# Kernel tuning notes

Measured on AMD Instinct MI355X. Metric: run time of the kernel, lower is better.

The kernel has to match this reference:

```python
import jax, jax.numpy as jnp
import numpy as np

D_K = 64  # head dim; scale = 1/sqrt(d_k)


def setup_inputs() -> dict:
    key = jax.random.key(0)
    kq, kk, kv = jax.random.split(key, 3)
    B, N, M = 16, 2048, 2048
    q = jax.random.normal(kq, (B, N, D_K), dtype=jnp.float32)
    k = jax.random.normal(kk, (B, M, D_K), dtype=jnp.float32)
    v = jax.random.normal(kv, (B, M, D_K), dtype=jnp.float32)
    return {"q": q, "k": k, "v": v}


def reference(q, k, v):
    # attn = softmax(q @ k^T / sqrt(d_k)); dropout is identity in eval mode
    scale = 1.0 / jnp.sqrt(jnp.asarray(D_K, dtype=q.dtype))
    scores = jnp.einsum("bnd,bmd->bnm", q, k) * scale  # (B, n, m)
    attn = jax.nn.softmax(scores, axis=2)
    out = jnp.einsum("bnm,bmd->bnd", attn, v)  # (B, n, d_v)
    return (out, attn)
```

## Files before the change

kernel.cpp:

```cpp
#include <hip/hip_runtime.h>

#define B_ 16
#define N_ 2048
#define M_ 2048
#define D_ 64

typedef short sv8 __attribute__((ext_vector_type(8)));
typedef short sv4 __attribute__((ext_vector_type(4)));
typedef float fv4 __attribute__((ext_vector_type(4)));

__device__ __forceinline__ short f2bf(float x) {
    union { float f; unsigned u; } a; a.f = x;
    unsigned r = a.u + 0x7FFFu + ((a.u >> 16) & 1u);
    return (short)(r >> 16);
}
__device__ __forceinline__ float bf2f(short s) {
    union { float f; unsigned u; } a;
    a.u = ((unsigned)(unsigned short)s) << 16;
    return a.f;
}

__device__ __forceinline__ int pidx(int r, int m) {
    return (r << 11) + ((((m >> 3) ^ (r & 7))) << 3) + (m & 7);
}

__global__ void conv_bf16(const float* __restrict__ in, short* __restrict__ outb) {
    int i = (blockIdx.x * 256 + threadIdx.x) * 4;
    float4 f = *(const float4*)(in + i);
    sv4 o; o[0] = f2bf(f.x); o[1] = f2bf(f.y); o[2] = f2bf(f.z); o[3] = f2bf(f.w);
    *(sv4*)(outb + i) = o;
}

__global__ void conv_vt(const float* __restrict__ v, short* __restrict__ vt) {
    __shared__ short tile[64][65];
    int t = threadIdx.x;
    int b = blockIdx.x >> 5;
    int mt = (blockIdx.x & 31) << 6;
    for (int i = 0; i < 4; ++i) {
        int idx = i * 256 + t;
        int m = idx >> 4;
        int dq = (idx & 15) << 2;
        float4 f = *(const float4*)(v + ((size_t)(b * M_ + mt + m) * D_ + dq));
        tile[m][dq + 0] = f2bf(f.x); tile[m][dq + 1] = f2bf(f.y);
        tile[m][dq + 2] = f2bf(f.z); tile[m][dq + 3] = f2bf(f.w);
    }
    __syncthreads();
    for (int j = 0; j < 2; ++j) {
        int idx = j * 256 + t;
        int d = idx >> 3;
        int mq = (idx & 7) << 3;
        sv4 o0, o1;
        #pragma unroll
        for (int c = 0; c < 4; ++c) o0[c] = tile[mq + c][d];
        #pragma unroll
        for (int c = 0; c < 4; ++c) o1[c] = tile[mq + 4 + c][d];
        short* dst = vt + ((size_t)(b * D_ + d) * M_ + mt + mq);
        *(sv4*)(dst) = o0;
        *(sv4*)(dst + 4) = o1;
    }
}

__global__ __launch_bounds__(256, 2) void attn_main(
    const short* __restrict__ Qb, const short* __restrict__ Kb,
    const short* __restrict__ Vt, float* __restrict__ outp,
    float* __restrict__ attnp)
{
    __shared__ short P[16 * 2048];
    __shared__ float l_sh[4][16];
    __shared__ float rinv_sh[16];

    const int tid = threadIdx.x;
    const int w = tid >> 6;
    const int lane = tid & 63;
    const int r = lane & 15;
    const int g = lane >> 4;

    const int b = blockIdx.x >> 7;
    const int n0 = (blockIdx.x & 127) << 4;

    const short* qbase = Qb + ((b * N_ + n0 + r) * D_ + g * 8);
    sv8 q0 = *(const sv8*)(qbase);
    sv8 q1 = *(const sv8*)(qbase + 32);

    float lpart = 0.f;

    for (int m0 = w * 16; m0 < M_; m0 += 64) {
        const short* kbase = Kb + ((b * M_ + m0 + r) * D_ + g * 8);
        sv8 a0 = *(const sv8*)(kbase);
        sv8 a1 = *(const sv8*)(kbase + 32);
        fv4 acc = {0.f, 0.f, 0.f, 0.f};
        acc = __builtin_amdgcn_mfma_f32_16x16x32_bf16(a0, q0, acc, 0, 0, 0);
        acc = __builtin_amdgcn_mfma_f32_16x16x32_bf16(a1, q1, acc, 0, 0, 0);
        float p0 = __expf(fminf(acc[0] * 0.125f, 80.f));
        float p1 = __expf(fminf(acc[1] * 0.125f, 80.f));
        float p2 = __expf(fminf(acc[2] * 0.125f, 80.f));
        float p3 = __expf(fminf(acc[3] * 0.125f, 80.f));
        lpart += (p0 + p1) + (p2 + p3);
        sv4 pw; pw[0] = f2bf(p0); pw[1] = f2bf(p1); pw[2] = f2bf(p2); pw[3] = f2bf(p3);
        *(sv4*)&P[pidx(r, m0 + g * 4)] = pw;
    }

    lpart += __shfl_xor(lpart, 16, 64);
    lpart += __shfl_xor(lpart, 32, 64);
    if (g == 0) l_sh[w][r] = lpart;
    __syncthreads();
    if (tid < 16) {
        float s = l_sh[0][tid] + l_sh[1][tid] + l_sh[2][tid] + l_sh[3][tid];
        rinv_sh[tid] = 1.f / s;
    }
    __syncthreads();

    const int base_row = b * N_ + n0;
    for (int i = 0; i < 32; ++i) {
        int idx = i * 256 + tid;
        int rr = idx >> 9;
        int mq = (idx & 511) << 2;
        sv4 pv = *(const sv4*)&P[pidx(rr, mq)];
        float ri = rinv_sh[rr];
        float4 o;
        o.x = bf2f(pv[0]) * ri; o.y = bf2f(pv[1]) * ri;
        o.z = bf2f(pv[2]) * ri; o.w = bf2f(pv[3]) * ri;
        *(float4*)(attnp + ((size_t)(base_row + rr) * M_ + mq)) = o;
    }

    fv4 acc = {0.f, 0.f, 0.f, 0.f};
    const short* vbase = Vt + ((size_t)(b * D_ + w * 16 + r) * M_);
    for (int m0 = 0; m0 < M_; m0 += 32) {
        sv8 pa = *(const sv8*)&P[pidx(r, m0 + g * 8)];
        sv8 vb = *(const sv8*)(vbase + m0 + g * 8);
        acc = __builtin_amdgcn_mfma_f32_16x16x32_bf16(pa, vb, acc, 0, 0, 0);
    }
    #pragma unroll
    for (int reg = 0; reg < 4; ++reg) {
        int nr = g * 4 + reg;
        outp[(size_t)(base_row + nr) * D_ + w * 16 + r] = acc[reg] * rinv_sh[nr];
    }
}

extern "C" void kernel_launch(void* const* d_in, const int* in_sizes, int n_in,
                              void* d_out, int out_size, void* d_ws, size_t ws_size,
                              hipStream_t stream) {
    const float* q = (const float*)d_in[0];
    const float* k = (const float*)d_in[1];
    const float* v = (const float*)d_in[2];
    float* outp = (float*)d_out;
    float* attnp = outp + (size_t)B_ * N_ * D_;

    short* Qb = (short*)d_ws;
    short* Kb = Qb + (size_t)B_ * N_ * D_;
    short* Vt = Kb + (size_t)B_ * M_ * D_;

    conv_bf16<<<2048, 256, 0, stream>>>(q, Qb);
    conv_bf16<<<2048, 256, 0, stream>>>(k, Kb);
    conv_vt<<<512, 256, 0, stream>>>(v, Vt);
    attn_main<<<B_ * (N_ / 16), 256, 0, stream>>>(Qb, Kb, Vt, outp, attnp);
}
```

Before: 156.5 us.

## Split attention into row-sum pass and streaming bulk pass with small per-wave LDS tiles

Replaces the single kernel, which buffered a whole 16x2048 probability row block in LDS, with two kernels. The first recomputes QK^T to get the softmax denominators. The second recomputes the scores and streams normalized attention and P@V in 64-column chunks through small double-buffered per-wave LDS tiles, using nontemporal stores. This cuts LDS use so more blocks fit per CU and lets attention-matrix writes interleave with compute, at the cost of computing QK^T twice. It also switches bf16 conversion to the hardware packed-convert instruction and drops the exp clamp.

```diff
diff --git a/kernel.cpp b/kernel.cpp
--- a/kernel.cpp
+++ b/kernel.cpp
@@ -4,6 +4,7 @@
 #define N_ 2048
 #define M_ 2048
 #define D_ 64
+#define SCALE 0.125f
 
 typedef short sv8 __attribute__((ext_vector_type(8)));
 typedef short sv4 __attribute__((ext_vector_type(4)));
@@ -14,21 +15,19 @@
     unsigned r = a.u + 0x7FFFu + ((a.u >> 16) & 1u);
     return (short)(r >> 16);
 }
-__device__ __forceinline__ float bf2f(short s) {
-    union { float f; unsigned u; } a;
-    a.u = ((unsigned)(unsigned short)s) << 16;
-    return a.f;
-}
-
-__device__ __forceinline__ int pidx(int r, int m) {
-    return (r << 11) + ((((m >> 3) ^ (r & 7))) << 3) + (m & 7);
-}
+__device__ __forceinline__ unsigned cvtpk(float lo, float hi) {
+    unsigned r;
+    asm("v_cvt_pk_bf16_f32 %0, %1, %2" : "=v"(r) : "v"(lo), "v"(hi));
+    return r;
+}
+__device__ __forceinline__ float bflo(unsigned u) { return __uint_as_float(u << 16); }
+__device__ __forceinline__ float bfhi(unsigned u) { return __uint_as_float(u & 0xffff0000u); }
 
 __global__ void conv_bf16(const float* __restrict__ in, short* __restrict__ outb) {
     int i = (blockIdx.x * 256 + threadIdx.x) * 4;
     float4 f = *(const float4*)(in + i);
-    sv4 o; o[0] = f2bf(f.x); o[1] = f2bf(f.y); o[2] = f2bf(f.z); o[3] = f2bf(f.w);
-    *(sv4*)(outb + i) = o;
+    uint2 o; o.x = cvtpk(f.x, f.y); o.y = cvtpk(f.z, f.w);
+    *(uint2*)(outb + i) = o;
 }
 
 __global__ void conv_vt(const float* __restrict__ v, short* __restrict__ vt) {
@@ -60,80 +59,127 @@
     }
 }
 
-__global__ __launch_bounds__(256, 2) void attn_main(
+__global__ __launch_bounds__(256) void attn_sums(
     const short* __restrict__ Qb, const short* __restrict__ Kb,
-    const short* __restrict__ Vt, float* __restrict__ outp,
-    float* __restrict__ attnp)
+    float* __restrict__ rinv_g)
 {
-    __shared__ short P[16 * 2048];
-    __shared__ float l_sh[4][16];
-    __shared__ float rinv_sh[16];
-
     const int tid = threadIdx.x;
-    const int w = tid >> 6;
-    const int lane = tid & 63;
-    const int r = lane & 15;
-    const int g = lane >> 4;
-
-    const int b = blockIdx.x >> 7;
-    const int n0 = (blockIdx.x & 127) << 4;
+    const int w = tid >> 6, lane = tid & 63;
+    const int r = lane & 15, g = lane >> 4;
+    const int b = blockIdx.x >> 5;
+    const int n0 = ((blockIdx.x & 31) << 6) + (w << 4);
 
     const short* qbase = Qb + ((b * N_ + n0 + r) * D_ + g * 8);
     sv8 q0 = *(const sv8*)(qbase);
     sv8 q1 = *(const sv8*)(qbase + 32);
-
-    float lpart = 0.f;
-
-    for (int m0 = w * 16; m0 < M_; m0 += 64) {
-        const short* kbase = Kb + ((b * M_ + m0 + r) * D_ + g * 8);
-        sv8 a0 = *(const sv8*)(kbase);
-        sv8 a1 = *(const sv8*)(kbase + 32);
-        fv4 acc = {0.f, 0.f, 0.f, 0.f};
-        acc = __builtin_amdgcn_mfma_f32_16x16x32_bf16(a0, q0, acc, 0, 0, 0);
-        acc = __builtin_amdgcn_mfma_f32_16x16x32_bf16(a1, q1, acc, 0, 0, 0);
-        float p0 = __expf(fminf(acc[0] * 0.125f, 80.f));
-        float p1 = __expf(fminf(acc[1] * 0.125f, 80.f));
-        float p2 = __expf(fminf(acc[2] * 0.125f, 80.f));
-        float p3 = __expf(fminf(acc[3] * 0.125f, 80.f));
-        lpart += (p0 + p1) + (p2 + p3);
-        sv4 pw; pw[0] = f2bf(p0); pw[1] = f2bf(p1); pw[2] = f2bf(p2); pw[3] = f2bf(p3);
-        *(sv4*)&P[pidx(r, m0 + g * 4)] = pw;
-    }
-
-    lpart += __shfl_xor(lpart, 16, 64);
-    lpart += __shfl_xor(lpart, 32, 64);
-    if (g == 0) l_sh[w][r] = lpart;
-    __syncthreads();
-    if (tid < 16) {
-        float s = l_sh[0][tid] + l_sh[1][tid] + l_sh[2][tid] + l_sh[3][tid];
-        rinv_sh[tid] = 1.f / s;
-    }
-    __syncthreads();
-
-    const int base_row = b * N_ + n0;
-    for (int i = 0; i < 32; ++i) {
-        int idx = i * 256 + tid;
-        int rr = idx >> 9;
-        int mq = (idx & 511) << 2;
-        sv4 pv = *(const sv4*)&P[pidx(rr, mq)];
-        float ri = rinv_sh[rr];
-        float4 o;
-        o.x = bf2f(pv[0]) * ri; o.y = bf2f(pv[1]) * ri;
-        o.z = bf2f(pv[2]) * ri; o.w = bf2f(pv[3]) * ri;
-        *(float4*)(attnp + ((size_t)(base_row + rr) * M_ + mq)) = o;
-    }
-
-    fv4 acc = {0.f, 0.f, 0.f, 0.f};
-    const short* vbase = Vt + ((size_t)(b * D_ + w * 16 + r) * M_);
-    for (int m0 = 0; m0 < M_; m0 += 32) {
-        sv8 pa = *(const sv8*)&P[pidx(r, m0 + g * 8)];
-        sv8 vb = *(const sv8*)(vbase + m0 + g * 8);
-        acc = __builtin_amdgcn_mfma_f32_16x16x32_bf16(pa, vb, acc, 0, 0, 0);
-    }
+    const short* kbb = Kb + (size_t)b * M_ * D_;
+
+    float lsum = 0.f;
+    for (int m0 = 0; m0 < M_; m0 += 64) {
+        #pragma unroll
+        for (int s = 0; s < 4; ++s) {
+            const short* ka = kbb + (m0 + s * 16 + r) * D_ + g * 8;
+            sv8 k0 = *(const sv8*)ka;
+            sv8 k1 = *(const sv8*)(ka + 32);
+            fv4 acc = {0.f, 0.f, 0.f, 0.f};
+            acc = __builtin_amdgcn_mfma_f32_16x16x32_bf16(k0, q0, acc, 0, 0, 0);
+            acc = __builtin_amdgcn_mfma_f32_16x16x32_bf16(k1, q1, acc, 0, 0, 0);
+            lsum += __expf(acc[0] * SCALE) + __expf(acc[1] * SCALE)
+                  + __expf(acc[2] * SCALE) + __expf(acc[3] * SCALE);
+        }
+    }
+    lsum += __shfl_xor(lsum, 16, 64);
+    lsum += __shfl_xor(lsum, 32, 64);
+    if (g == 0) rinv_g[b * N_ + n0 + r] = 1.f / lsum;
+}
+
+__global__ __launch_bounds__(256) void attn_bulk(
+    const short* __restrict__ Qb, const short* __restrict__ Kb,
+    const short* __restrict__ Vt, const float* __restrict__ rinv_g,
+    float* __restrict__ outp, float* __restrict__ attnp)
+{
+    __shared__ short Pt[4][2][1024];
+
+    const int tid = threadIdx.x;
+    const int w = tid >> 6, lane = tid & 63;
+    const int r = lane & 15, g = lane >> 4;
+    const int b = blockIdx.x >> 5;
+    const int n0 = ((blockIdx.x & 31) << 6) + (w << 4);
+
+    const short* qbase = Qb + ((b * N_ + n0 + r) * D_ + g * 8);
+    sv8 q0 = *(const sv8*)(qbase);
+    sv8 q1 = *(const sv8*)(qbase + 32);
+
+    float rinv = rinv_g[b * N_ + n0 + r];
+    const int n_st = lane >> 2, mq = lane & 3;
+    float rinv_st = __shfl(rinv, n_st, 64);
+
+    char* lds = (char*)&Pt[w][0][0];
+
+    int wb[4], ra[2], ab[4];
+    #pragma unroll
+    for (int s = 0; s < 4; ++s)
+        wb[s] = r * 128 + (((s * 2 + (g >> 1)) ^ (r & 7)) << 4) + ((g & 1) * 8);
+    #pragma unroll
+    for (int c = 0; c < 2; ++c)
+        ra[c] = r * 128 + (((c * 4 + g) ^ (r & 7)) << 4);
+    #pragma unroll
+    for (int c2 = 0; c2 < 4; ++c2)
+        ab[c2] = n_st * 128 + (((c2 * 2 + (mq >> 1)) ^ (n_st & 7)) << 4) + ((mq & 1) * 8);
+
+    fv4 ac0 = {0.f,0.f,0.f,0.f}, ac1 = {0.f,0.f,0.f,0.f};
+    fv4 ac2 = {0.f,0.f,0.f,0.f}, ac3 = {0.f,0.f,0.f,0.f};
+
+    const short* kbb = Kb + (size_t)b * M_ * D_;
+    const short* vbb = Vt + (size_t)b * D_ * M_;
+    float* arow = attnp + (size_t)(b * N_ + n0 + n_st) * M_ + mq * 4;
+
+    int buf = 0;
+    for (int m0 = 0; m0 < M_; m0 += 64, buf ^= 1) {
+        char* ldsb = lds + (buf << 11);
+
+        #pragma unroll
+        for (int s = 0; s < 4; ++s) {
+            const short* ka = kbb + (m0 + s * 16 + r) * D_ + g * 8;
+            sv8 k0 = *(const sv8*)ka;
+            sv8 k1 = *(const sv8*)(ka + 32);
+            fv4 acc = {0.f, 0.f, 0.f, 0.f};
+            acc = __builtin_amdgcn_mfma_f32_16x16x32_bf16(k0, q0, acc, 0, 0, 0);
+            acc = __builtin_amdgcn_mfma_f32_16x16x32_bf16(k1, q1, acc, 0, 0, 0);
+            float p0 = __expf(acc[0] * SCALE), p1 = __expf(acc[1] * SCALE);
+            float p2 = __expf(acc[2] * SCALE), p3 = __expf(acc[3] * SCALE);
+            uint2 pk; pk.x = cvtpk(p0, p1); pk.y = cvtpk(p2, p3);
+            *(uint2*)(ldsb + wb[s]) = pk;
+        }
+
+        #pragma unroll
+        for (int c2 = 0; c2 < 4; ++c2) {
+            uint2 pv = *(const uint2*)(ldsb + ab[c2]);
+            fv4 o;
+            o[0] = bflo(pv.x) * rinv_st; o[1] = bfhi(pv.x) * rinv_st;
+            o[2] = bflo(pv.y) * rinv_st; o[3] = bfhi(pv.y) * rinv_st;
+            __builtin_nontemporal_store(o, (fv4*)(arow + m0 + c2 * 16));
+        }
+
+        #pragma unroll
+        for (int c = 0; c < 2; ++c) {
+            sv8 pa = *(const sv8*)(ldsb + ra[c]);
+            const short* vb0 = vbb + r * M_ + m0 + c * 32 + g * 8;
+            ac0 = __builtin_amdgcn_mfma_f32_16x16x32_bf16(pa, *(const sv8*)(vb0),            ac0, 0, 0, 0);
+            ac1 = __builtin_amdgcn_mfma_f32_16x16x32_bf16(pa, *(const sv8*)(vb0 + 16 * M_), ac1, 0, 0, 0);
+            ac2 = __builtin_amdgcn_mfma_f32_16x16x32_bf16(pa, *(const sv8*)(vb0 + 32 * M_), ac2, 0, 0, 0);
+            ac3 = __builtin_amdgcn_mfma_f32_16x16x32_bf16(pa, *(const sv8*)(vb0 + 48 * M_), ac3, 0, 0, 0);
+        }
+    }
+
+    float* obase = outp + (size_t)(b * N_ + n0 + g * 4) * D_ + r;
     #pragma unroll
     for (int reg = 0; reg < 4; ++reg) {
-        int nr = g * 4 + reg;
-        outp[(size_t)(base_row + nr) * D_ + w * 16 + r] = acc[reg] * rinv_sh[nr];
+        float ri = __shfl(rinv, g * 4 + reg, 64);
+        __builtin_nontemporal_store(ac0[reg] * ri, obase + reg * D_);
+        __builtin_nontemporal_store(ac1[reg] * ri, obase + reg * D_ + 16);
+        __builtin_nontemporal_store(ac2[reg] * ri, obase + reg * D_ + 32);
+        __builtin_nontemporal_store(ac3[reg] * ri, obase + reg * D_ + 48);
     }
 }
 
@@ -149,9 +195,11 @@
     short* Qb = (short*)d_ws;
     short* Kb = Qb + (size_t)B_ * N_ * D_;
     short* Vt = Kb + (size_t)B_ * M_ * D_;
+    float* rinv_g = (float*)(Vt + (size_t)B_ * M_ * D_);
 
     conv_bf16<<<2048, 256, 0, stream>>>(q, Qb);
     conv_bf16<<<2048, 256, 0, stream>>>(k, Kb);
     conv_vt<<<512, 256, 0, stream>>>(v, Vt);
-    attn_main<<<B_ * (N_ / 16), 256, 0, stream>>>(Qb, Kb, Vt, outp, attnp);
-}
+    attn_sums<<<512, 256, 0, stream>>>(Qb, Kb, rinv_g);
+    attn_bulk<<<512, 256, 0, stream>>>(Qb, Kb, Vt, rinv_g, outp, attnp);
+}
```

After: 201.0 us. 28.5% more time.
